# Kernel tuning notes

Hardware: AMD Instinct MI355X
Metric: run time of the kernel (lower is better)

The kernel has to match this reference:

```python
import jax, jax.numpy as jnp
import numpy as np

EPS = 1e-8

def correlation_map(a, b):
    # a, b: (N, C, H, W). L2-normalize features along channel, then dense correlation.
    a = a / (jnp.linalg.norm(a, axis=1, keepdims=True) + EPS)
    b = b / (jnp.linalg.norm(b, axis=1, keepdims=True) + EPS)
    # corr[n, i, j, x, y] = <a[n,:,i,j], b[n,:,x,y]>
    return jnp.einsum('nchw,ncxy->nhwxy', a, b)


def setup_inputs() -> dict:
    key = jax.random.key(0)
    k1, k2, k3, k4 = jax.random.split(key, 4)
    N, C, H, W = 4, 64, 64, 64
    return {
        'featsA': jax.random.normal(k1, (N, C, H, W), dtype=jnp.float32),
        'warpedA': jax.random.normal(k2, (N, C, H, W), dtype=jnp.float32),
        'tensorB': jax.random.normal(k3, (N, C, H, W), dtype=jnp.float32),
        'warp_grid': jax.random.uniform(k4, (N, H, W, 2), dtype=jnp.float32),
        'patch_size': 9,
    }


def reference(featsA, warpedA, tensorB, warp_grid, patch_size):
    # featsA and warp_grid are accepted (as in the original signature) but unused by the loss.
    corr = correlation_map(warpedA, tensorB)  # (N, H, W, H, W)
    N, H, W = corr.shape[0], corr.shape[1], corr.shape[2]
    hp = (patch_size - 1) // 2
    ci = jnp.arange(hp, H - hp)              # interior row centers (Hi,)
    cj = jnp.arange(hp, W - hp)              # interior col centers (Wj,)
    d = jnp.arange(patch_size) - hp          # window offsets (ps,)
    I = ci[:, None, None, None]              # (Hi,1,1,1)
    J = cj[None, :, None, None]              # (1,Wj,1,1)
    # For interior (i,j), the rolled boolean window selects the ps x ps block of the
    # last two dims centered at (i,j) (no wrap-around for interior centers), row-major.
    patches = corr[:, I, J, I + d[None, None, :, None], J + d[None, None, None, :]]
    # patches: (N, Hi, Wj, ps, ps)
    flat = patches.reshape(N, ci.shape[0], cj.shape[0], patch_size * patch_size)
    logp = jax.nn.log_softmax(flat, axis=-1)
    return -jnp.sum(logp)
```

## Files before the change

### kernel.cpp

```cpp
#include <hip/hip_runtime.h>

typedef short  bf16x8 __attribute__((ext_vector_type(8)));
typedef float  f32x4  __attribute__((ext_vector_type(4)));

#define HP 4

__global__ __launch_bounds__(256) void fused_kernel(const float* __restrict__ A,
                                                    const float* __restrict__ B,
                                                    float* __restrict__ partials) {
    __shared__ ushort bt[9][64][72];
    __shared__ ushort at[64][72];
    __shared__ float  binv[9][64];
    __shared__ float  ainv_s[64];
    __shared__ float  red[16];

    const int b0 = blockIdx.x;
    const int b  = (b0 & 7) * 28 + (b0 >> 3);
    const int n  = b / 56;
    const int i  = b - n * 56 + HP;
    const int t  = threadIdx.x, wib = t >> 6, l = t & 63;

    for (int rr = 0; rr < 3; ++rr) {
        const int r = wib + rr * 4;
        if (r > 9) break;
        const int hrow = (r == 9) ? i : (i - HP + r);
        const float* src = ((r == 9) ? A : B) + (size_t)n * 262144 + (size_t)hrow * 64 + l;
        ushort* dst = ((r == 9) ? &at[0][0] : &bt[r][0][0]) + l * 72;
        float ss = 0.f;
        #pragma unroll
        for (int c0 = 0; c0 < 64; c0 += 8) {
            float v[8];
            #pragma unroll
            for (int q = 0; q < 8; ++q) v[q] = src[(size_t)(c0 + q) * 4096];
            uint pk[4];
            #pragma unroll
            for (int q = 0; q < 4; ++q) {
                ss += v[2*q] * v[2*q] + v[2*q+1] * v[2*q+1];
                uint u0 = __float_as_uint(v[2*q]);   u0 = (u0 + 0x7FFFu + ((u0 >> 16) & 1)) >> 16;
                uint u1 = __float_as_uint(v[2*q+1]); u1 = (u1 + 0x7FFFu + ((u1 >> 16) & 1)) >> 16;
                pk[q] = u0 | (u1 << 16);
            }
            *(uint4*)(dst + c0) = *(const uint4*)pk;
        }
        const float inv = 1.0f / (sqrtf(ss) + 1e-8f);
        if (r == 9) ainv_s[l] = inv; else binv[r][l] = inv;
    }
    __syncthreads();

    const int lo = l & 15, hi = l >> 4;
    const int j0 = HP + wib * 16;
    const int arow_l = min(j0 + lo, 63);
    const bf16x8 a0 = *(const bf16x8*)&at[arow_l][hi * 8];
    const bf16x8 a1 = *(const bf16x8*)&at[arow_l][hi * 8 + 32];

    int jrow[4]; float av[4];
    #pragma unroll
    for (int r = 0; r < 4; ++r) {
        jrow[r] = j0 + hi * 4 + r;
        av[r]   = ainv_s[min(jrow[r], 63)];
    }

    float s_acc[4]  = {0.f, 0.f, 0.f, 0.f};
    float sx_acc[4] = {0.f, 0.f, 0.f, 0.f};

    #pragma unroll
    for (int ti = 0; ti < 2; ++ti) {
        const int ntv = wib + ti;
        if (ntv > 3) break;
        const int col = ntv * 16 + lo;
        float vm[4];
        #pragma unroll
        for (int r = 0; r < 4; ++r) {
            int d = col - jrow[r];
            vm[r] = (jrow[r] < 60 && d >= -HP && d <= HP) ? 1.0f : 0.0f;
        }
        #pragma unroll
        for (int di = 0; di < 9; ++di) {
            const ushort* q = &bt[di][col][hi * 8];
            const bf16x8 bq0 = *(const bf16x8*)q;
            const bf16x8 bq1 = *(const bf16x8*)(q + 32);
            f32x4 acc = __builtin_amdgcn_mfma_f32_16x16x32_bf16(a0, bq0,
                            (f32x4){0.f, 0.f, 0.f, 0.f}, 0, 0, 0);
            acc = __builtin_amdgcn_mfma_f32_16x16x32_bf16(a1, bq1, acc, 0, 0, 0);
            const float bi = binv[di][col];
            #pragma unroll
            for (int r = 0; r < 4; ++r) {
                float p = acc[r] * (av[r] * bi);
                float e = __expf(p);
                s_acc[r]  = fmaf(vm[r], e, s_acc[r]);
                sx_acc[r] = fmaf(vm[r], p, sx_acc[r]);
            }
        }
    }

    #pragma unroll
    for (int r = 0; r < 4; ++r) {
        #pragma unroll
        for (int off = 1; off < 16; off <<= 1) {
            s_acc[r]  += __shfl_xor(s_acc[r],  off);
            sx_acc[r] += __shfl_xor(sx_acc[r], off);
        }
    }
    if (lo == 0) {
        float csum = 0.f;
        #pragma unroll
        for (int r = 0; r < 4; ++r)
            if (jrow[r] < 60) csum += 81.0f * __logf(s_acc[r]) - sx_acc[r];
        red[wib * 4 + hi] = csum;
    }
    __syncthreads();
    if (t == 0) {
        float t2 = 0.f;
        #pragma unroll
        for (int k = 0; k < 16; ++k) t2 += red[k];
        partials[b] = t2;
    }
}

__global__ __launch_bounds__(64) void reduce_kernel(const float* __restrict__ partials,
                                                    float* __restrict__ out) {
    const int t = threadIdx.x;
    float s = 0.f;
    #pragma unroll
    for (int k = 0; k < 4; ++k) {
        int idx = k * 64 + t;
        if (idx < 224) s += partials[idx];
    }
    #pragma unroll
    for (int off = 32; off; off >>= 1) s += __shfl_xor(s, off);
    if (t == 0) out[0] = s;
}

extern "C" void kernel_launch(void* const* d_in, const int* in_sizes, int n_in,
                              void* d_out, int out_size, void* d_ws, size_t ws_size,
                              hipStream_t stream) {
    const float* warpedA = (const float*)d_in[1];
    const float* tensorB = (const float*)d_in[2];
    float* partials = (float*)d_ws;
    float* out = (float*)d_out;

    fused_kernel<<<224, 256, 0, stream>>>(warpedA, tensorB, partials);
    reduce_kernel<<<1, 64, 0, stream>>>(partials, out);
}
```

Before: 15.76 us.

## Fuse final reduction into main kernel via sentinel slots and widen blocks to ten waves

The separate reduce kernel is removed. Each block publishes its partial sum as a sentinel-tagged 64-bit slot, and block 0 spins until all slots are ready, sums them and clears them. Blocks grow to 640 threads so each of ten waves loads one row with all 64 channel loads in flight, and eight waves each take one MFMA tile instead of four waves doing two. This saves a kernel launch and adds load-level parallelism, but it depends on every block making forward progress while block 0 spins, and the larger register and thread footprint may limit occupancy.

```diff
diff --git a/kernel.cpp b/kernel.cpp
--- a/kernel.cpp
+++ b/kernel.cpp
@@ -4,15 +4,18 @@
 typedef float  f32x4  __attribute__((ext_vector_type(4)));
 
 #define HP 4
+#define SENT 0x5F3C2A1Du
 
-__global__ __launch_bounds__(256) void fused_kernel(const float* __restrict__ A,
+__global__ __launch_bounds__(640) void fused_kernel(const float* __restrict__ A,
                                                     const float* __restrict__ B,
-                                                    float* __restrict__ partials) {
+                                                    unsigned long long* __restrict__ slots,
+                                                    float* __restrict__ out) {
     __shared__ ushort bt[9][64][72];
     __shared__ ushort at[64][72];
     __shared__ float  binv[9][64];
     __shared__ float  ainv_s[64];
-    __shared__ float  red[16];
+    __shared__ float  s_lds[8][16];
+    __shared__ float  sx_lds[8][16];
 
     const int b0 = blockIdx.x;
     const int b  = (b0 & 7) * 28 + (b0 >> 3);
@@ -20,115 +23,144 @@
     const int i  = b - n * 56 + HP;
     const int t  = threadIdx.x, wib = t >> 6, l = t & 63;
 
-    for (int rr = 0; rr < 3; ++rr) {
-        const int r = wib + rr * 4;
-        if (r > 9) break;
+    {
+        const int r = wib;
         const int hrow = (r == 9) ? i : (i - HP + r);
         const float* src = ((r == 9) ? A : B) + (size_t)n * 262144 + (size_t)hrow * 64 + l;
         ushort* dst = ((r == 9) ? &at[0][0] : &bt[r][0][0]) + l * 72;
-        float ss = 0.f;
+
+        float v[64];
+        #pragma unroll
+        for (int c = 0; c < 64; ++c) v[c] = src[(size_t)c * 4096];
+
+        float ss0 = 0.f, ss1 = 0.f, ss2 = 0.f, ss3 = 0.f;
+        #pragma unroll
+        for (int c = 0; c < 64; c += 4) {
+            ss0 = fmaf(v[c],   v[c],   ss0);
+            ss1 = fmaf(v[c+1], v[c+1], ss1);
+            ss2 = fmaf(v[c+2], v[c+2], ss2);
+            ss3 = fmaf(v[c+3], v[c+3], ss3);
+        }
         #pragma unroll
         for (int c0 = 0; c0 < 64; c0 += 8) {
-            float v[8];
-            #pragma unroll
-            for (int q = 0; q < 8; ++q) v[q] = src[(size_t)(c0 + q) * 4096];
             uint pk[4];
             #pragma unroll
             for (int q = 0; q < 4; ++q) {
-                ss += v[2*q] * v[2*q] + v[2*q+1] * v[2*q+1];
-                uint u0 = __float_as_uint(v[2*q]);   u0 = (u0 + 0x7FFFu + ((u0 >> 16) & 1)) >> 16;
-                uint u1 = __float_as_uint(v[2*q+1]); u1 = (u1 + 0x7FFFu + ((u1 >> 16) & 1)) >> 16;
+                uint u0 = __float_as_uint(v[c0 + 2*q]);     u0 = (u0 + 0x7FFFu + ((u0 >> 16) & 1)) >> 16;
+                uint u1 = __float_as_uint(v[c0 + 2*q + 1]); u1 = (u1 + 0x7FFFu + ((u1 >> 16) & 1)) >> 16;
                 pk[q] = u0 | (u1 << 16);
             }
             *(uint4*)(dst + c0) = *(const uint4*)pk;
         }
-        const float inv = 1.0f / (sqrtf(ss) + 1e-8f);
+        const float inv = 1.0f / (sqrtf((ss0 + ss1) + (ss2 + ss3)) + 1e-8f);
         if (r == 9) ainv_s[l] = inv; else binv[r][l] = inv;
     }
     __syncthreads();
 
     const int lo = l & 15, hi = l >> 4;
-    const int j0 = HP + wib * 16;
-    const int arow_l = min(j0 + lo, 63);
-    const bf16x8 a0 = *(const bf16x8*)&at[arow_l][hi * 8];
-    const bf16x8 a1 = *(const bf16x8*)&at[arow_l][hi * 8 + 32];
+    if (wib < 8) {
+        const int m   = wib & 3, ti = wib >> 2;
+        const int ntv = m + ti;
+        const int j0  = HP + m * 16;
+        const int arow_l = min(j0 + lo, 63);
+        const bf16x8 a0 = *(const bf16x8*)&at[arow_l][hi * 8];
+        const bf16x8 a1 = *(const bf16x8*)&at[arow_l][hi * 8 + 32];
 
-    int jrow[4]; float av[4];
-    #pragma unroll
-    for (int r = 0; r < 4; ++r) {
-        jrow[r] = j0 + hi * 4 + r;
-        av[r]   = ainv_s[min(jrow[r], 63)];
-    }
-
-    float s_acc[4]  = {0.f, 0.f, 0.f, 0.f};
-    float sx_acc[4] = {0.f, 0.f, 0.f, 0.f};
-
-    #pragma unroll
-    for (int ti = 0; ti < 2; ++ti) {
-        const int ntv = wib + ti;
-        if (ntv > 3) break;
-        const int col = ntv * 16 + lo;
-        float vm[4];
+        int jrow[4]; float av[4];
         #pragma unroll
         for (int r = 0; r < 4; ++r) {
-            int d = col - jrow[r];
-            vm[r] = (jrow[r] < 60 && d >= -HP && d <= HP) ? 1.0f : 0.0f;
+            jrow[r] = j0 + hi * 4 + r;
+            av[r]   = ainv_s[min(jrow[r], 63)];
+        }
+
+        float s_acc[4]  = {0.f, 0.f, 0.f, 0.f};
+        float sx_acc[4] = {0.f, 0.f, 0.f, 0.f};
+
+        if (ntv < 4) {
+            const int col = ntv * 16 + lo;
+            float vm[4];
+            #pragma unroll
+            for (int r = 0; r < 4; ++r) {
+                int d = col - jrow[r];
+                vm[r] = (jrow[r] < 60 && d >= -HP && d <= HP) ? 1.0f : 0.0f;
+            }
+            #pragma unroll
+            for (int di = 0; di < 9; ++di) {
+                const ushort* q = &bt[di][col][hi * 8];
+                const bf16x8 bq0 = *(const bf16x8*)q;
+                const bf16x8 bq1 = *(const bf16x8*)(q + 32);
+                f32x4 acc = __builtin_amdgcn_mfma_f32_16x16x32_bf16(a0, bq0,
+                                (f32x4){0.f, 0.f, 0.f, 0.f}, 0, 0, 0);
+                acc = __builtin_amdgcn_mfma_f32_16x16x32_bf16(a1, bq1, acc, 0, 0, 0);
+                const float bi = binv[di][col];
+                #pragma unroll
+                for (int r = 0; r < 4; ++r) {
+                    float p = acc[r] * (av[r] * bi);
+                    float e = __expf(p);
+                    s_acc[r]  = fmaf(vm[r], e, s_acc[r]);
+                    sx_acc[r] = fmaf(vm[r], p, sx_acc[r]);
+                }
+            }
         }
         #pragma unroll
-        for (int di = 0; di < 9; ++di) {
-            const ushort* q = &bt[di][col][hi * 8];
-            const bf16x8 bq0 = *(const bf16x8*)q;
-            const bf16x8 bq1 = *(const bf16x8*)(q + 32);
-            f32x4 acc = __builtin_amdgcn_mfma_f32_16x16x32_bf16(a0, bq0,
-                            (f32x4){0.f, 0.f, 0.f, 0.f}, 0, 0, 0);
-            acc = __builtin_amdgcn_mfma_f32_16x16x32_bf16(a1, bq1, acc, 0, 0, 0);
-            const float bi = binv[di][col];
+        for (int r = 0; r < 4; ++r) {
+            #pragma unroll
+            for (int off = 1; off < 16; off <<= 1) {
+                s_acc[r]  += __shfl_xor(s_acc[r],  off);
+                sx_acc[r] += __shfl_xor(sx_acc[r], off);
+            }
+        }
+        if (lo == 0) {
             #pragma unroll
             for (int r = 0; r < 4; ++r) {
-                float p = acc[r] * (av[r] * bi);
-                float e = __expf(p);
-                s_acc[r]  = fmaf(vm[r], e, s_acc[r]);
-                sx_acc[r] = fmaf(vm[r], p, sx_acc[r]);
+                s_lds[wib][hi * 4 + r]  = s_acc[r];
+                sx_lds[wib][hi * 4 + r] = sx_acc[r];
             }
         }
     }
+    __syncthreads();
 
-    #pragma unroll
-    for (int r = 0; r < 4; ++r) {
+    if (wib == 0) {
+        const int m2 = l >> 4, rib = l & 15;
+        float contrib = 0.f;
+        if (l < 56) {
+            float s  = s_lds[m2][rib]  + s_lds[m2 + 4][rib];
+            float sx = sx_lds[m2][rib] + sx_lds[m2 + 4][rib];
+            contrib = 81.0f * __logf(s) - sx;
+        }
         #pragma unroll
-        for (int off = 1; off < 16; off <<= 1) {
-            s_acc[r]  += __shfl_xor(s_acc[r],  off);
-            sx_acc[r] += __shfl_xor(sx_acc[r], off);
+        for (int off = 32; off; off >>= 1) contrib += __shfl_xor(contrib, off);
+        if (l == 0) {
+            unsigned long long payload =
+                ((unsigned long long)SENT << 32) | (unsigned long long)__float_as_uint(contrib);
+            __hip_atomic_store(&slots[b], payload, __ATOMIC_RELAXED, __HIP_MEMORY_SCOPE_AGENT);
+        }
+        if (b == 0) {
+            float s = 0.f;
+            #pragma unroll
+            for (int k = 0; k < 4; ++k) {
+                const int idx = k * 64 + l;
+                if (idx < 224) {
+                    unsigned long long v;
+                    for (;;) {
+                        v = __hip_atomic_load(&slots[idx], __ATOMIC_RELAXED, __HIP_MEMORY_SCOPE_AGENT);
+                        if ((v >> 32) == (unsigned long long)SENT) break;
+                        __builtin_amdgcn_s_sleep(1);
+                    }
+                    s += __uint_as_float((unsigned int)v);
+                }
+            }
+            #pragma unroll
+            for (int off = 32; off; off >>= 1) s += __shfl_xor(s, off);
+            #pragma unroll
+            for (int k = 0; k < 4; ++k) {
+                const int idx = k * 64 + l;
+                if (idx < 224)
+                    __hip_atomic_store(&slots[idx], 0ull, __ATOMIC_RELAXED, __HIP_MEMORY_SCOPE_AGENT);
+            }
+            if (l == 0) out[0] = s;
         }
     }
-    if (lo == 0) {
-        float csum = 0.f;
-        #pragma unroll
-        for (int r = 0; r < 4; ++r)
-            if (jrow[r] < 60) csum += 81.0f * __logf(s_acc[r]) - sx_acc[r];
-        red[wib * 4 + hi] = csum;
-    }
-    __syncthreads();
-    if (t == 0) {
-        float t2 = 0.f;
-        #pragma unroll
-        for (int k = 0; k < 16; ++k) t2 += red[k];
-        partials[b] = t2;
-    }
-}
-
-__global__ __launch_bounds__(64) void reduce_kernel(const float* __restrict__ partials,
-                                                    float* __restrict__ out) {
-    const int t = threadIdx.x;
-    float s = 0.f;
-    #pragma unroll
-    for (int k = 0; k < 4; ++k) {
-        int idx = k * 64 + t;
-        if (idx < 224) s += partials[idx];
-    }
-    #pragma unroll
-    for (int off = 32; off; off >>= 1) s += __shfl_xor(s, off);
-    if (t == 0) out[0] = s;
 }
 
 extern "C" void kernel_launch(void* const* d_in, const int* in_sizes, int n_in,
@@ -136,9 +168,8 @@
                               hipStream_t stream) {
     const float* warpedA = (const float*)d_in[1];
     const float* tensorB = (const float*)d_in[2];
-    float* partials = (float*)d_ws;
+    unsigned long long* slots = (unsigned long long*)d_ws;
     float* out = (float*)d_out;
 
-    fused_kernel<<<224, 256, 0, stream>>>(warpedA, tensorB, partials);
-    reduce_kernel<<<1, 64, 0, stream>>>(partials, out);
+    fused_kernel<<<224, 640, 0, stream>>>(warpedA, tensorB, slots, out);
 }
```

After: 16.54 us. 1.05x slower.
